# Performance work log

Hardware: AMD Instinct MI355X
Metric: run time of the kernel (lower is better)

The kernel has to match this reference:

```python
import jax, jax.numpy as jnp
import numpy as np

NUM_CLASSES = 21
THRESHOLD = 0.5
VAR0, VAR1 = 0.1, 0.2
NEGPOS_RATIO = 3


def setup_inputs() -> dict:
    key = jax.random.key(0)
    k1, k2, k3, k4, k5, k6, k7 = jax.random.split(key, 7)
    B, P, C, O = 64, 8732, 21, 8
    loc_data = jax.random.normal(k1, (B, P, 4), dtype=jnp.float32) * 0.1
    conf_data = jax.random.normal(k2, (B, P, C), dtype=jnp.float32)
    # priors: center form (cx, cy, w, h), valid in [0,1]
    cxy = jax.random.uniform(k3, (P, 2), minval=0.05, maxval=0.95)
    pwh = jax.random.uniform(k4, (P, 2), minval=0.05, maxval=0.3)
    priors = jnp.concatenate([cxy, pwh], axis=-1).astype(jnp.float32)
    # targets: corner-form boxes + class label (float), (B, O, 5)
    tc = jax.random.uniform(k5, (B, O, 2), minval=0.2, maxval=0.8)
    twh = jax.random.uniform(k6, (B, O, 2), minval=0.1, maxval=0.4)
    tmin = jnp.clip(tc - twh / 2, 0.0, 1.0)
    tmax = jnp.clip(tc + twh / 2, 0.0, 1.0)
    labels = jax.random.randint(k7, (B, O, 1), 0, C - 1).astype(jnp.float32)
    targets = jnp.concatenate([tmin, tmax, labels], axis=-1)
    return {"loc_data": loc_data, "conf_data": conf_data, "priors": priors, "targets": targets}


def _point_form(p):
    # (cx,cy,w,h) -> (xmin,ymin,xmax,ymax)
    return jnp.concatenate([p[:, :2] - p[:, 2:] / 2, p[:, :2] + p[:, 2:] / 2], axis=-1)


def _jaccard(a, b):
    # a: (O,4) corners, b: (P,4) corners -> (O,P)
    lt = jnp.maximum(a[:, None, :2], b[None, :, :2])
    rb = jnp.minimum(a[:, None, 2:], b[None, :, 2:])
    wh = jnp.clip(rb - lt, 0.0, None)
    inter = wh[..., 0] * wh[..., 1]
    area_a = ((a[:, 2] - a[:, 0]) * (a[:, 3] - a[:, 1]))[:, None]
    area_b = ((b[:, 2] - b[:, 0]) * (b[:, 3] - b[:, 1]))[None, :]
    return inter / (area_a + area_b - inter)


def _match_one(truths, labels, priors_pt, priors):
    # truths: (O,4) corners, labels: (O,), priors: (P,4) center-form
    ov = _jaccard(truths, priors_pt)                      # (O,P)
    best_prior_idx = jnp.argmax(ov, axis=1)               # (O,)
    best_truth_overlap = jnp.max(ov, axis=0)              # (P,)
    best_truth_idx = jnp.argmax(ov, axis=0)               # (P,)
    # ensure every gt box matches its best prior
    best_truth_overlap = best_truth_overlap.at[best_prior_idx].set(2.0)
    best_truth_idx = best_truth_idx.at[best_prior_idx].set(jnp.arange(truths.shape[0]))
    matched = truths[best_truth_idx]                      # (P,4)
    conf = labels[best_truth_idx].astype(jnp.int32) + 1
    conf = jnp.where(best_truth_overlap < THRESHOLD, 0, conf)
    # encode offsets
    g_cxcy = ((matched[:, :2] + matched[:, 2:]) / 2 - priors[:, :2]) / (VAR0 * priors[:, 2:])
    g_wh = jnp.log(jnp.clip((matched[:, 2:] - matched[:, :2]) / priors[:, 2:], 1e-8, None)) / VAR1
    return jnp.concatenate([g_cxcy, g_wh], axis=-1), conf


def _forward(loc_data, conf_data, priors, targets):
    B, P, C = conf_data.shape
    priors_sg = jax.lax.stop_gradient(priors)             # torch uses .data
    targets_sg = jax.lax.stop_gradient(targets)
    priors_pt = _point_form(priors_sg)
    loc_t, conf_t = jax.vmap(_match_one, in_axes=(0, 0, None, None))(
        targets_sg[:, :, :4], targets_sg[:, :, 4], priors_pt, priors_sg)
    pos = conf_t > 0                                      # (B,P)

    # localization: smooth L1 summed over positive priors
    diff = loc_data - loc_t
    ad = jnp.abs(diff)
    sl1 = jnp.where(ad < 1.0, 0.5 * diff * diff, ad - 0.5)
    loss_l = jnp.sum(sl1 * pos[..., None].astype(sl1.dtype))

    # per-prior conf loss for hard negative mining
    lse = jax.nn.logsumexp(conf_data, axis=-1)            # (B,P)
    gathered = jnp.take_along_axis(conf_data, conf_t[..., None], axis=-1)[..., 0]
    loss_c_all = lse - gathered                           # (B,P)
    mined = jnp.where(pos, 0.0, loss_c_all)
    loss_idx = jnp.argsort(-mined, axis=1)                # descending
    idx_rank = jnp.argsort(loss_idx, axis=1)
    num_pos = jnp.sum(pos.astype(jnp.int32), axis=1, keepdims=True)  # (B,1)
    num_neg = jnp.minimum(NEGPOS_RATIO * num_pos, P - num_pos)
    neg = idx_rank < num_neg                              # (B,P)

    sel = (pos | neg).astype(loss_c_all.dtype)
    loss_c = jnp.sum(loss_c_all * sel)

    N = jnp.sum(num_pos).astype(loss_l.dtype)
    return loss_l / N, loss_c / N


def reference(loc_data, conf_data, priors, targets):
    return _forward(loc_data, conf_data, priors, targets)
```

## Files before the change

### kernel.cpp

```cpp
#include <hip/hip_runtime.h>
#include <math.h>

#define TPB 256
#define TPBS 1024
#define LDSF 12288
#define HP 17

typedef unsigned long long ull;
typedef float pf4 __attribute__((ext_vector_type(4), aligned(4)));

__device__ __forceinline__ float jac(float tx0, float ty0, float tx1, float ty1, float ta,
                                     float px0, float py0, float px1, float py1, float pa) {
    float ltx = fmaxf(tx0, px0), lty = fmaxf(ty0, py0);
    float rbx = fminf(tx1, px1), rby = fminf(ty1, py1);
    float w = fmaxf(rbx - ltx, 0.0f), h = fmaxf(rby - lty, 0.0f);
    float inter = w * h;
    return inter / (ta + pa - inter);
}

template <int ON, int CN>
__global__ __launch_bounds__(TPB) void fused_kernel(
    const float* __restrict__ loc, const float* __restrict__ priors,
    const float* __restrict__ targets, const float* __restrict__ conf,
    int P, int O_rt, int C_rt, int CB2,
    float* __restrict__ mined, ull* __restrict__ pkeys,
    float* __restrict__ part_ll, float* __restrict__ part_pc,
    int* __restrict__ part_np) {
    constexpr int OMAX = (ON > 0) ? ON : 64;
    constexpr int CC = (CN > 0) ? CN : 32;
    const int O = (ON > 0) ? ON : O_rt;
    const int C = (CN > 0) ? CN : C_rt;
    const int b = blockIdx.x / CB2;
    const int chunk = blockIdx.x % CB2;
    const int tid = threadIdx.x;
    const int p = chunk * TPB + tid;
    const bool pv = (p < P);
    const int lane = tid & 63, wv = tid >> 6;

    __shared__ float s_tx0[OMAX], s_ty0[OMAX], s_tx1[OMAX], s_ty1[OMAX];
    __shared__ float s_lab[OMAX], s_area[OMAX];
    __shared__ ull s_wk[TPB / 64][OMAX];
    __shared__ float s_wll[TPB / 64], s_wpc[TPB / 64];
    __shared__ int s_wnp[TPB / 64];

    float rv[CC];
    float4 pr4 = make_float4(0.f, 0.f, 1.f, 1.f);
    if (pv) {
        const float* row = conf + ((size_t)b * P + p) * C;
        if (CN > 0) {
#pragma unroll
            for (int q = 0; q < CN / 4; ++q) {
                pf4 v = *(const pf4*)(row + 4 * q);
#pragma unroll
                for (int e = 0; e < 4; ++e) rv[4 * q + e] = v[e];
            }
#pragma unroll
            for (int j = (CN / 4) * 4; j < CN; ++j) rv[j] = row[j];
        } else {
            for (int j = 0; j < C; ++j) rv[j] = row[j];
        }
        pr4 = ((const float4*)priors)[p];
    }

    for (int o = tid; o < O; o += TPB) {
        const float* t = targets + ((size_t)b * O + o) * 5;
        float x0 = t[0], y0 = t[1], x1 = t[2], y1 = t[3];
        s_tx0[o] = x0; s_ty0[o] = y0; s_tx1[o] = x1; s_ty1[o] = y1;
        s_lab[o] = t[4];
        s_area[o] = (x1 - x0) * (y1 - y0);
    }
    __syncthreads();

    float cx = pr4.x, cy = pr4.y, pw = pr4.z, ph = pr4.w;
    float px0 = cx - pw * 0.5f, py0 = cy - ph * 0.5f;
    float px1 = cx + pw * 0.5f, py1 = cy + ph * 0.5f;
    float pa = (px1 - px0) * (py1 - py0);
    float bto = -1.0f;
    int bti = 0;
    for (int o = 0; o < O; ++o) {
        float ov = -1.0f;
        if (pv) {
            ov = jac(s_tx0[o], s_ty0[o], s_tx1[o], s_ty1[o], s_area[o],
                     px0, py0, px1, py1, pa);
            if (ov > bto) { bto = ov; bti = o; }
        }
        float mx = ov;
#pragma unroll
        for (int d = 1; d < 64; d <<= 1)
            mx = fmaxf(mx, __shfl_xor(mx, d, 64));
        ull kk = 0ull;
        if (mx >= 0.0f) {
            ull msk = __ballot(ov == mx);
            int src = __ffsll(msk) - 1;
            unsigned pw_ = (unsigned)(chunk * TPB + (wv << 6) + src);
            kk = ((ull)__float_as_uint(mx) << 32) | (ull)(0xFFFFFFFFu - pw_);
        }
        if (lane == 0) s_wk[wv][o] = kk;
    }
    __syncthreads();
    if (tid < O) {
        ull kk = s_wk[0][tid];
        for (int w = 1; w < TPB / 64; ++w)
            if (s_wk[w][tid] > kk) kk = s_wk[w][tid];
        pkeys[((size_t)b * O + tid) * CB2 + chunk] = kk;
    }

    float ll = 0.0f, pc = 0.0f;
    int np = 0;
    if (pv) {
        float m = rv[0];
#pragma unroll
        for (int j = 1; j < CC; ++j) { if (CN > 0 || j < C) m = fmaxf(m, rv[j]); }
        float s = 0.0f;
#pragma unroll
        for (int j = 0; j < CC; ++j) { if (CN > 0 || j < C) s += __expf(rv[j] - m); }
        float lse = m + __logf(s);

        int c = (bto < 0.5f) ? 0 : ((int)s_lab[bti] + 1);
        float rowc = rv[0];
#pragma unroll
        for (int j = 1; j < CC; ++j) { if (CN > 0 || j < C) { if (c == j) rowc = rv[j]; } }
        float lc = lse - rowc;

        bool pos = c > 0;
        mined[(size_t)b * P + p] = pos ? 0.0f : lc;
        if (pos) {
            pc = lc;
            np = 1;
            float mx0 = s_tx0[bti], my0 = s_ty0[bti];
            float mx1 = s_tx1[bti], my1 = s_ty1[bti];
            float g0 = ((mx0 + mx1) * 0.5f - cx) / (0.1f * pw);
            float g1 = ((my0 + my1) * 0.5f - cy) / (0.1f * ph);
            float g2 = logf(fmaxf((mx1 - mx0) / pw, 1e-8f)) / 0.2f;
            float g3 = logf(fmaxf((my1 - my0) / ph, 1e-8f)) / 0.2f;
            float4 ld = ((const float4*)loc)[(size_t)b * P + p];
            float gt4[4] = {g0, g1, g2, g3};
            float lv[4] = {ld.x, ld.y, ld.z, ld.w};
#pragma unroll
            for (int q = 0; q < 4; ++q) {
                float d = lv[q] - gt4[q];
                float ad = fabsf(d);
                ll += (ad < 1.0f) ? 0.5f * d * d : (ad - 0.5f);
            }
        }
    }

#pragma unroll
    for (int d = 1; d < 64; d <<= 1) {
        ll += __shfl_xor(ll, d, 64);
        pc += __shfl_xor(pc, d, 64);
        np += __shfl_xor(np, d, 64);
    }
    if (lane == 0) { s_wll[wv] = ll; s_wpc[wv] = pc; s_wnp[wv] = np; }
    __syncthreads();
    if (tid == 0) {
        float L = 0.f, Pc = 0.f;
        int N = 0;
        for (int w = 0; w < TPB / 64; ++w) { L += s_wll[w]; Pc += s_wpc[w]; N += s_wnp[w]; }
        part_ll[blockIdx.x] = L;
        part_pc[blockIdx.x] = Pc;
        part_np[blockIdx.x] = N;
    }
}

template <int ON, int CN>
__global__ __launch_bounds__(TPBS) void select_kernel(
    const float* __restrict__ mined, const float* __restrict__ conf,
    const float* __restrict__ loc, const float* __restrict__ priors,
    const float* __restrict__ targets, const ull* __restrict__ pkeys,
    const float* __restrict__ part_ll, const float* __restrict__ part_pc,
    const int* __restrict__ part_np,
    float* __restrict__ ll_batch, float* __restrict__ lc_batch,
    int* __restrict__ np_batch,
    int P, int O_rt, int C_rt, int CB2, int ratio) {
    constexpr int OMAX = (ON > 0) ? ON : 64;
    constexpr int NV = LDSF / TPBS;
    const int O = (ON > 0) ? ON : O_rt;
    const int C = (CN > 0) ? CN : C_rt;
    const int b = blockIdx.x, tid = threadIdx.x;
    const int lane = tid & 63, wv = tid >> 6;
    constexpr int W = TPBS / 64;
    const float* v = mined + (size_t)b * P;
    const bool reg = (P <= NV * TPBS);

    __shared__ int s_hist[256 * HP];
    __shared__ float s_tx0[OMAX], s_ty0[OMAX], s_tx1[OMAX], s_ty1[OMAX];
    __shared__ float s_lab[OMAX], s_area[OMAX];
    __shared__ ull s_keys[OMAX];
    __shared__ int s_bp[OMAX];
    __shared__ float s_wf[W], s_wg[W];
    __shared__ int s_wi[W];
    __shared__ int s_wt[4];
    __shared__ unsigned s_bsel;
    __shared__ int s_krn;
    __shared__ float s_bc[2], s_fix[2];
    __shared__ int s_bn, s_fixn;

    float val[NV];
#pragma unroll
    for (int j = 0; j < NV; ++j) {
        int i = tid + j * TPBS;
        val[j] = (reg && i < P) ? v[i] : 0.0f;
    }

    float pll = 0.0f, ppc = 0.0f;
    int pnp = 0;
    for (int i = tid; i < CB2; i += TPBS) {
        pll += part_ll[b * CB2 + i];
        ppc += part_pc[b * CB2 + i];
        pnp += part_np[b * CB2 + i];
    }
#pragma unroll
    for (int d = 1; d < 64; d <<= 1) {
        pll += __shfl_xor(pll, d, 64);
        ppc += __shfl_xor(ppc, d, 64);
        pnp += __shfl_xor(pnp, d, 64);
    }
    if (lane == 0) { s_wf[wv] = pll; s_wg[wv] = ppc; s_wi[wv] = pnp; }

    if (tid < O) {
        const float* t = targets + ((size_t)b * O + tid) * 5;
        float x0 = t[0], y0 = t[1], x1 = t[2], y1 = t[3];
        s_tx0[tid] = x0; s_ty0[tid] = y0; s_tx1[tid] = x1; s_ty1[tid] = y1;
        s_lab[tid] = t[4];
        s_area[tid] = (x1 - x0) * (y1 - y0);
        s_keys[tid] = 0ull;
    }
    __syncthreads();

    for (int i = tid; i < O * CB2; i += TPBS) {
        int o = i / CB2, s = i % CB2;
        atomicMax(&s_keys[o], pkeys[((size_t)b * O + o) * CB2 + s]);
    }
    __syncthreads();
    if (tid < O)
        s_bp[tid] = (int)(0xFFFFFFFFu - (unsigned)(s_keys[tid] & 0xFFFFFFFFull));
    __syncthreads();

    if (reg) {
#pragma unroll
        for (int j = 0; j < NV; ++j) {
            int i = tid + j * TPBS;
            bool z = false;
            for (int o = 0; o < O; ++o) z |= (s_bp[o] == i);
            if (z) val[j] = 0.0f;
        }
    }
    unsigned uvv[NV];
#pragma unroll
    for (int j = 0; j < NV; ++j) uvv[j] = __float_as_uint(val[j]);

    float dll = 0.0f, dpc = 0.0f;
    int dnp = 0;
    if (tid < O) {
        const int o = tid;
        const int p = s_bp[o];
        bool owner = true;
        for (int o2 = o + 1; o2 < O; ++o2)
            if (s_bp[o2] == p) owner = false;
        if (owner) {
            float4 pr = ((const float4*)priors)[p];
            float cx = pr.x, cy = pr.y, pw = pr.z, ph = pr.w;
            float px0 = cx - pw * 0.5f, py0 = cy - ph * 0.5f;
            float px1 = cx + pw * 0.5f, py1 = cy + ph * 0.5f;
            float pa = (px1 - px0) * (py1 - py0);
            float bto = -1.0f;
            int bti = 0;
            for (int o2 = 0; o2 < O; ++o2) {
                float ov = jac(s_tx0[o2], s_ty0[o2], s_tx1[o2], s_ty1[o2], s_area[o2],
                               px0, py0, px1, py1, pa);
                if (ov > bto) { bto = ov; bti = o2; }
            }
            int c_t = (bto < 0.5f) ? 0 : ((int)s_lab[bti] + 1);
            const float* row = conf + ((size_t)b * P + p) * C;
            float m = row[0];
            for (int j = 1; j < C; ++j) m = fmaxf(m, row[j]);
            float s = 0.0f;
            for (int j = 0; j < C; ++j) s += __expf(row[j] - m);
            float lse = m + __logf(s);
            int c_n = (int)s_lab[o] + 1;
            float lc_n = lse - row[c_n];
            bool pos_t = c_t > 0;
            float lc_t = lse - row[c_t];
            dpc = lc_n - (pos_t ? lc_t : 0.0f);
            dnp = 1 - (pos_t ? 1 : 0);
            float4 ld = ((const float4*)loc)[(size_t)b * P + p];
            float lv[4] = {ld.x, ld.y, ld.z, ld.w};
            float sl_new = 0.0f, sl_old = 0.0f;
            {
                float mx0 = s_tx0[o], my0 = s_ty0[o], mx1 = s_tx1[o], my1 = s_ty1[o];
                float g[4] = {((mx0 + mx1) * 0.5f - cx) / (0.1f * pw),
                              ((my0 + my1) * 0.5f - cy) / (0.1f * ph),
                              logf(fmaxf((mx1 - mx0) / pw, 1e-8f)) / 0.2f,
                              logf(fmaxf((my1 - my0) / ph, 1e-8f)) / 0.2f};
                for (int q = 0; q < 4; ++q) {
                    float d = lv[q] - g[q];
                    float ad = fabsf(d);
                    sl_new += (ad < 1.0f) ? 0.5f * d * d : (ad - 0.5f);
                }
            }
            if (pos_t) {
                float mx0 = s_tx0[bti], my0 = s_ty0[bti], mx1 = s_tx1[bti], my1 = s_ty1[bti];
                float g[4] = {((mx0 + mx1) * 0.5f - cx) / (0.1f * pw),
                              ((my0 + my1) * 0.5f - cy) / (0.1f * ph),
                              logf(fmaxf((mx1 - mx0) / pw, 1e-8f)) / 0.2f,
                              logf(fmaxf((my1 - my0) / ph, 1e-8f)) / 0.2f};
                for (int q = 0; q < 4; ++q) {
                    float d = lv[q] - g[q];
                    float ad = fabsf(d);
                    sl_old += (ad < 1.0f) ? 0.5f * d * d : (ad - 0.5f);
                }
            }
            dll = sl_new - sl_old;
        }
    }
    if (wv == 0) {
#pragma unroll
        for (int d = 1; d < 64; d <<= 1) {
            dll += __shfl_xor(dll, d, 64);
            dpc += __shfl_xor(dpc, d, 64);
            dnp += __shfl_xor(dnp, d, 64);
        }
        if (lane == 0) { s_fix[0] = dll; s_fix[1] = dpc; s_fixn = dnp; }
    }
    __syncthreads();
    if (tid == 0) {
        float L = 0.f, Pc = 0.f;
        int N = 0;
        for (int w = 0; w < W; ++w) { L += s_wf[w]; Pc += s_wg[w]; N += s_wi[w]; }
        s_bc[0] = L + s_fix[0]; s_bc[1] = Pc + s_fix[1]; s_bn = N + s_fixn;
    }
    __syncthreads();
    const float ll_sum = s_bc[0];
    const float sum_pos = s_bc[1];
    const int npos = s_bn;

    const int k = min(ratio * npos, P - npos);
    if (tid == 0) {
        ll_batch[b] = ll_sum;
        np_batch[b] = npos;
    }
    if (k <= 0) {
        if (tid == 0) lc_batch[b] = sum_pos;
        return;
    }

    unsigned prefix = 0u;
    int kr = k;
    for (int pass = 0; pass < 4; ++pass) {
        const int shift = 24 - 8 * pass;
        const unsigned mask = (pass == 0) ? 0u : (0xFFFFFFFFu << (32 - 8 * pass));
        for (int i = tid; i < 256 * HP; i += TPBS) s_hist[i] = 0;
        __syncthreads();
        if (reg) {
#pragma unroll
            for (int j = 0; j < NV; ++j) {
                int i = tid + j * TPBS;
                unsigned u = uvv[j];
                bool match = (i < P) && ((u & mask) == prefix);
                int bin = (u >> shift) & 0xFF;
                if (pass == 0) {
                    ull act = __ballot(match);
                    while (act) {
                        int src = __ffsll(act) - 1;
                        int b0 = __shfl(bin, src, 64);
                        ull same = __ballot(match && bin == b0) & act;
                        if (lane == src)
                            atomicAdd(&s_hist[b0 * HP + wv], (int)__popcll(same));
                        act &= ~same;
                    }
                } else if (match) {
                    atomicAdd(&s_hist[bin * HP + wv], 1);
                }
            }
        } else {
            for (int i = tid; i < P; i += TPBS) {
                float x = v[i];
                for (int o = 0; o < O; ++o)
                    if (i == s_bp[o]) x = 0.0f;
                unsigned u = __float_as_uint(x);
                bool match = ((u & mask) == prefix);
                int bin = (u >> shift) & 0xFF;
                if (pass == 0) {
                    ull act = __ballot(match);
                    while (act) {
                        int src = __ffsll(act) - 1;
                        int b0 = __shfl(bin, src, 64);
                        ull same = __ballot(match && bin == b0) & act;
                        if (lane == src)
                            atomicAdd(&s_hist[b0 * HP + wv], (int)__popcll(same));
                        act &= ~same;
                    }
                } else if (match) {
                    atomicAdd(&s_hist[bin * HP + wv], 1);
                }
            }
        }
        __syncthreads();
        int sge = 0, h = 0;
        if (tid < 256) {
            for (int w = 0; w < W; ++w) h += s_hist[tid * HP + w];
            int val_ = h;
#pragma unroll
            for (int d = 1; d < 64; d <<= 1) {
                int t = __shfl_down(val_, d, 64);
                if (lane + d < 64) val_ += t;
            }
            if (lane == 0) s_wt[tid >> 6] = val_;
            sge = val_;
        }
        __syncthreads();
        if (tid < 256) {
            for (int w = (tid >> 6) + 1; w < 4; ++w) sge += s_wt[w];
            int sgt = sge - h;
            if (sge >= kr && sgt < kr) {
                s_bsel = (unsigned)tid;
                s_krn = kr - sgt;
            }
        }
        __syncthreads();
        prefix |= s_bsel << shift;
        kr = s_krn;
    }
    const float T = __uint_as_float(prefix);
    float lsum = 0.0f;
    int lcnt = 0;
    if (reg) {
#pragma unroll
        for (int j = 0; j < NV; ++j) {
            int i = tid + j * TPBS;
            if (i < P && val[j] > T) { lsum += val[j]; ++lcnt; }
        }
    } else {
        for (int i = tid; i < P; i += TPBS) {
            float x = v[i];
            for (int o = 0; o < O; ++o)
                if (i == s_bp[o]) x = 0.0f;
            if (x > T) { lsum += x; ++lcnt; }
        }
    }
#pragma unroll
    for (int d = 1; d < 64; d <<= 1) {
        lsum += __shfl_xor(lsum, d, 64);
        lcnt += __shfl_xor(lcnt, d, 64);
    }
    if (lane == 0) { s_wf[wv] = lsum; s_wi[wv] = lcnt; }
    __syncthreads();
    if (tid == 0) {
        float S = 0.f;
        int Cn = 0;
        for (int w = 0; w < W; ++w) { S += s_wf[w]; Cn += s_wi[w]; }
        lc_batch[b] = sum_pos + S + (float)(k - Cn) * T;
    }
}

__global__ __launch_bounds__(TPB) void finalize_kernel(
    const float* __restrict__ ll_batch, const int* __restrict__ np_batch,
    const float* __restrict__ lc_batch, int B, float* __restrict__ out) {
    const int tid = threadIdx.x;
    __shared__ float s_l[TPB], s_c[TPB];
    __shared__ int s_n[TPB];
    float l = 0.0f, c = 0.0f;
    int n = 0;
    for (int i = tid; i < B; i += TPB) {
        l += ll_batch[i];
        c += lc_batch[i];
        n += np_batch[i];
    }
    s_l[tid] = l; s_c[tid] = c; s_n[tid] = n;
    __syncthreads();
    for (int s = TPB / 2; s > 0; s >>= 1) {
        if (tid < s) {
            s_l[tid] += s_l[tid + s];
            s_c[tid] += s_c[tid + s];
            s_n[tid] += s_n[tid + s];
        }
        __syncthreads();
    }
    if (tid == 0) {
        float N = (float)s_n[0];
        out[0] = s_l[0] / N;
        out[1] = s_c[0] / N;
    }
}

extern "C" void kernel_launch(void* const* d_in, const int* in_sizes, int n_in,
                              void* d_out, int out_size, void* d_ws, size_t ws_size,
                              hipStream_t stream) {
    const float* loc = (const float*)d_in[0];
    const float* conf = (const float*)d_in[1];
    const float* priors = (const float*)d_in[2];
    const float* targets = (const float*)d_in[3];

    const int P = in_sizes[2] / 4;
    const int B = in_sizes[0] / (P * 4);
    const int C = in_sizes[1] / (in_sizes[0] / 4);
    const int O = in_sizes[3] / (B * 5);
    const size_t BP = (size_t)B * P;
    const int CB2 = (P + TPB - 1) / TPB;

    ull* pkeys = (ull*)d_ws;
    float* mined = (float*)(pkeys + (size_t)B * O * CB2);
    float* part_ll = mined + BP;
    float* part_pc = part_ll + (size_t)B * CB2;
    int* part_np = (int*)(part_pc + (size_t)B * CB2);
    float* ll_batch = (float*)(part_np + (size_t)B * CB2);
    float* lc_batch = ll_batch + B;
    int* np_batch = (int*)(lc_batch + B);

    if (O == 8 && C == 21) {
        fused_kernel<8, 21><<<B * CB2, TPB, 0, stream>>>(
            loc, priors, targets, conf, P, O, C, CB2,
            mined, pkeys, part_ll, part_pc, part_np);
        select_kernel<8, 21><<<B, TPBS, 0, stream>>>(
            mined, conf, loc, priors, targets, pkeys, part_ll, part_pc, part_np,
            ll_batch, lc_batch, np_batch, P, O, C, CB2, 3);
    } else {
        fused_kernel<0, 0><<<B * CB2, TPB, 0, stream>>>(
            loc, priors, targets, conf, P, O, C, CB2,
            mined, pkeys, part_ll, part_pc, part_np);
        select_kernel<0, 0><<<B, TPBS, 0, stream>>>(
            mined, conf, loc, priors, targets, pkeys, part_ll, part_pc, part_np,
            ll_batch, lc_batch, np_batch, P, O, C, CB2, 3);
    }

    finalize_kernel<<<1, TPB, 0, stream>>>(ll_batch, np_batch, lc_batch, B,
                                           (float*)d_out);
}
```

Measured before the change: 118.8 us.

## Build first radix-select histogram in fused kernel and drop block key reduction

The fused kernel now builds the top-byte histogram of the mined loss for each 256-prior chunk. It packs each histogram as 16-bit pairs into a workspace buffer, and the select kernel sums these instead of doing pass 0 over all priors. Forced-match priors are fixed up in the histogram by moving one count to bin 0. The per-block max reduction of match keys is also removed: each wave writes its key directly and select reduces four times as many entries. Register-held values shrink from 12 to 9 per thread, and the per-wave padded histogram becomes a single shared histogram. This trades a 1024-thread serial pass for more global partial data and a CB2-long serial loop in select.

Result: no change. 117.9 us (-0.8%).

```diff
diff --git a/kernel.cpp b/kernel.cpp
--- a/kernel.cpp
+++ b/kernel.cpp
@@ -3,8 +3,7 @@
 
 #define TPB 256
 #define TPBS 1024
-#define LDSF 12288
-#define HP 17
+#define NVREG 9
 
 typedef unsigned long long ull;
 typedef float pf4 __attribute__((ext_vector_type(4), aligned(4)));
@@ -25,9 +24,10 @@
     int P, int O_rt, int C_rt, int CB2,
     float* __restrict__ mined, ull* __restrict__ pkeys,
     float* __restrict__ part_ll, float* __restrict__ part_pc,
-    int* __restrict__ part_np) {
+    int* __restrict__ part_np, unsigned* __restrict__ chist) {
     constexpr int OMAX = (ON > 0) ? ON : 64;
     constexpr int CC = (CN > 0) ? CN : 32;
+    constexpr int WPB = TPB / 64;
     const int O = (ON > 0) ? ON : O_rt;
     const int C = (CN > 0) ? CN : C_rt;
     const int b = blockIdx.x / CB2;
@@ -36,12 +36,13 @@
     const int p = chunk * TPB + tid;
     const bool pv = (p < P);
     const int lane = tid & 63, wv = tid >> 6;
+    const int CB2W = CB2 * WPB;
 
     __shared__ float s_tx0[OMAX], s_ty0[OMAX], s_tx1[OMAX], s_ty1[OMAX];
     __shared__ float s_lab[OMAX], s_area[OMAX];
-    __shared__ ull s_wk[TPB / 64][OMAX];
-    __shared__ float s_wll[TPB / 64], s_wpc[TPB / 64];
-    __shared__ int s_wnp[TPB / 64];
+    __shared__ int s_h[256];
+    __shared__ float s_wll[WPB], s_wpc[WPB];
+    __shared__ int s_wnp[WPB];
 
     float rv[CC];
     float4 pr4 = make_float4(0.f, 0.f, 1.f, 1.f);
@@ -62,6 +63,7 @@
         pr4 = ((const float4*)priors)[p];
     }
 
+    s_h[tid] = 0;
     for (int o = tid; o < O; o += TPB) {
         const float* t = targets + ((size_t)b * O + o) * 5;
         float x0 = t[0], y0 = t[1], x1 = t[2], y1 = t[3];
@@ -95,18 +97,14 @@
             unsigned pw_ = (unsigned)(chunk * TPB + (wv << 6) + src);
             kk = ((ull)__float_as_uint(mx) << 32) | (ull)(0xFFFFFFFFu - pw_);
         }
-        if (lane == 0) s_wk[wv][o] = kk;
-    }
-    __syncthreads();
-    if (tid < O) {
-        ull kk = s_wk[0][tid];
-        for (int w = 1; w < TPB / 64; ++w)
-            if (s_wk[w][tid] > kk) kk = s_wk[w][tid];
-        pkeys[((size_t)b * O + tid) * CB2 + chunk] = kk;
+        if (lane == 0)
+            pkeys[((size_t)b * O + o) * CB2W + chunk * WPB + wv] = kk;
     }
 
     float ll = 0.0f, pc = 0.0f;
     int np = 0;
+    int bin = 0;
+    bool hv = false;
     if (pv) {
         float m = rv[0];
 #pragma unroll
@@ -123,7 +121,10 @@
         float lc = lse - rowc;
 
         bool pos = c > 0;
-        mined[(size_t)b * P + p] = pos ? 0.0f : lc;
+        float mv = pos ? 0.0f : lc;
+        mined[(size_t)b * P + p] = mv;
+        bin = (int)(__float_as_uint(mv) >> 24);
+        hv = true;
         if (pos) {
             pc = lc;
             np = 1;
@@ -145,6 +146,17 @@
         }
     }
 
+    {
+        ull act = __ballot(hv);
+        while (act) {
+            int src = __ffsll(act) - 1;
+            int b0 = __shfl(bin, src, 64);
+            ull same = __ballot(hv && bin == b0) & act;
+            if (lane == src) atomicAdd(&s_h[b0], (int)__popcll(same));
+            act &= ~same;
+        }
+    }
+
 #pragma unroll
     for (int d = 1; d < 64; d <<= 1) {
         ll += __shfl_xor(ll, d, 64);
@@ -156,10 +168,14 @@
     if (tid == 0) {
         float L = 0.f, Pc = 0.f;
         int N = 0;
-        for (int w = 0; w < TPB / 64; ++w) { L += s_wll[w]; Pc += s_wpc[w]; N += s_wnp[w]; }
+        for (int w = 0; w < WPB; ++w) { L += s_wll[w]; Pc += s_wpc[w]; N += s_wnp[w]; }
         part_ll[blockIdx.x] = L;
         part_pc[blockIdx.x] = Pc;
         part_np[blockIdx.x] = N;
+    }
+    if (tid < 128) {
+        unsigned wd = (unsigned)s_h[2 * tid] | ((unsigned)s_h[2 * tid + 1] << 16);
+        chist[((size_t)b * CB2 + chunk) * 128 + tid] = wd;
     }
 }
 
@@ -169,21 +185,22 @@
     const float* __restrict__ loc, const float* __restrict__ priors,
     const float* __restrict__ targets, const ull* __restrict__ pkeys,
     const float* __restrict__ part_ll, const float* __restrict__ part_pc,
-    const int* __restrict__ part_np,
+    const int* __restrict__ part_np, const unsigned* __restrict__ chist,
     float* __restrict__ ll_batch, float* __restrict__ lc_batch,
     int* __restrict__ np_batch,
     int P, int O_rt, int C_rt, int CB2, int ratio) {
     constexpr int OMAX = (ON > 0) ? ON : 64;
-    constexpr int NV = LDSF / TPBS;
+    constexpr int NV = NVREG;
     const int O = (ON > 0) ? ON : O_rt;
     const int C = (CN > 0) ? CN : C_rt;
     const int b = blockIdx.x, tid = threadIdx.x;
     const int lane = tid & 63, wv = tid >> 6;
     constexpr int W = TPBS / 64;
+    const int CB2W = CB2 * (TPB / 64);
     const float* v = mined + (size_t)b * P;
     const bool reg = (P <= NV * TPBS);
 
-    __shared__ int s_hist[256 * HP];
+    __shared__ int s_hist[256];
     __shared__ float s_tx0[OMAX], s_ty0[OMAX], s_tx1[OMAX], s_ty1[OMAX];
     __shared__ float s_lab[OMAX], s_area[OMAX];
     __shared__ ull s_keys[OMAX];
@@ -228,9 +245,9 @@
     }
     __syncthreads();
 
-    for (int i = tid; i < O * CB2; i += TPBS) {
-        int o = i / CB2, s = i % CB2;
-        atomicMax(&s_keys[o], pkeys[((size_t)b * O + o) * CB2 + s]);
+    for (int i = tid; i < O * CB2W; i += TPBS) {
+        int o = i / CB2W, s = i % CB2W;
+        atomicMax(&s_keys[o], pkeys[((size_t)b * O + o) * CB2W + s]);
     }
     __syncthreads();
     if (tid < O)
@@ -250,8 +267,17 @@
 #pragma unroll
     for (int j = 0; j < NV; ++j) uvv[j] = __float_as_uint(val[j]);
 
+    if (tid < 256) {
+        int h = 0;
+        const unsigned* cb = chist + (size_t)b * CB2 * 128 + (tid >> 1);
+        const int sh = (tid & 1) * 16;
+        for (int c = 0; c < CB2; ++c) h += (int)((cb[c * 128] >> sh) & 0xFFFFu);
+        s_hist[tid] = h;
+    }
+
     float dll = 0.0f, dpc = 0.0f;
     int dnp = 0;
+    int adj_bin = -1;
     if (tid < O) {
         const int o = tid;
         const int p = s_bp[o];
@@ -259,6 +285,7 @@
         for (int o2 = o + 1; o2 < O; ++o2)
             if (s_bp[o2] == p) owner = false;
         if (owner) {
+            adj_bin = (int)(__float_as_uint(v[p]) >> 24);
             float4 pr = ((const float4*)priors)[p];
             float cx = pr.x, cy = pr.y, pw = pr.z, ph = pr.w;
             float px0 = cx - pw * 0.5f, py0 = cy - ph * 0.5f;
@@ -324,6 +351,10 @@
         if (lane == 0) { s_fix[0] = dll; s_fix[1] = dpc; s_fixn = dnp; }
     }
     __syncthreads();
+    if (adj_bin > 0) {
+        atomicAdd(&s_hist[adj_bin], -1);
+        atomicAdd(&s_hist[0], 1);
+    }
     if (tid == 0) {
         float L = 0.f, Pc = 0.f;
         int N = 0;
@@ -349,57 +380,33 @@
     int kr = k;
     for (int pass = 0; pass < 4; ++pass) {
         const int shift = 24 - 8 * pass;
-        const unsigned mask = (pass == 0) ? 0u : (0xFFFFFFFFu << (32 - 8 * pass));
-        for (int i = tid; i < 256 * HP; i += TPBS) s_hist[i] = 0;
-        __syncthreads();
-        if (reg) {
-#pragma unroll
-            for (int j = 0; j < NV; ++j) {
-                int i = tid + j * TPBS;
-                unsigned u = uvv[j];
-                bool match = (i < P) && ((u & mask) == prefix);
-                int bin = (u >> shift) & 0xFF;
-                if (pass == 0) {
-                    ull act = __ballot(match);
-                    while (act) {
-                        int src = __ffsll(act) - 1;
-                        int b0 = __shfl(bin, src, 64);
-                        ull same = __ballot(match && bin == b0) & act;
-                        if (lane == src)
-                            atomicAdd(&s_hist[b0 * HP + wv], (int)__popcll(same));
-                        act &= ~same;
-                    }
-                } else if (match) {
-                    atomicAdd(&s_hist[bin * HP + wv], 1);
+        if (pass > 0) {
+            const unsigned mask = 0xFFFFFFFFu << (32 - 8 * pass);
+            if (tid < 256) s_hist[tid] = 0;
+            __syncthreads();
+            if (reg) {
+#pragma unroll
+                for (int j = 0; j < NV; ++j) {
+                    int i = tid + j * TPBS;
+                    unsigned u = uvv[j];
+                    if (i < P && (u & mask) == prefix)
+                        atomicAdd(&s_hist[(u >> shift) & 0xFF], 1);
                 }
-            }
-        } else {
-            for (int i = tid; i < P; i += TPBS) {
-                float x = v[i];
-                for (int o = 0; o < O; ++o)
-                    if (i == s_bp[o]) x = 0.0f;
-                unsigned u = __float_as_uint(x);
-                bool match = ((u & mask) == prefix);
-                int bin = (u >> shift) & 0xFF;
-                if (pass == 0) {
-                    ull act = __ballot(match);
-                    while (act) {
-                        int src = __ffsll(act) - 1;
-                        int b0 = __shfl(bin, src, 64);
-                        ull same = __ballot(match && bin == b0) & act;
-                        if (lane == src)
-                            atomicAdd(&s_hist[b0 * HP + wv], (int)__popcll(same));
-                        act &= ~same;
-                    }
-                } else if (match) {
-                    atomicAdd(&s_hist[bin * HP + wv], 1);
+            } else {
+                for (int i = tid; i < P; i += TPBS) {
+                    float x = v[i];
+                    for (int o = 0; o < O; ++o)
+                        if (i == s_bp[o]) x = 0.0f;
+                    unsigned u = __float_as_uint(x);
+                    if ((u & mask) == prefix)
+                        atomicAdd(&s_hist[(u >> shift) & 0xFF], 1);
                 }
             }
-        }
-        __syncthreads();
+            __syncthreads();
+        }
         int sge = 0, h = 0;
         if (tid < 256) {
-            for (int w = 0; w < W; ++w) h += s_hist[tid * HP + w];
+            h = s_hist[tid];
             int val_ = h;
 #pragma unroll
             for (int d = 1; d < 64; d <<= 1) {
@@ -498,30 +505,32 @@
     const int O = in_sizes[3] / (B * 5);
     const size_t BP = (size_t)B * P;
     const int CB2 = (P + TPB - 1) / TPB;
+    const int CB2W = CB2 * (TPB / 64);
 
     ull* pkeys = (ull*)d_ws;
-    float* mined = (float*)(pkeys + (size_t)B * O * CB2);
+    float* mined = (float*)(pkeys + (size_t)B * O * CB2W);
     float* part_ll = mined + BP;
     float* part_pc = part_ll + (size_t)B * CB2;
     int* part_np = (int*)(part_pc + (size_t)B * CB2);
-    float* ll_batch = (float*)(part_np + (size_t)B * CB2);
+    unsigned* chist = (unsigned*)(part_np + (size_t)B * CB2);
+    float* ll_batch = (float*)(chist + (size_t)B * CB2 * 128);
     float* lc_batch = ll_batch + B;
     int* np_batch = (int*)(lc_batch + B);
 
     if (O == 8 && C == 21) {
         fused_kernel<8, 21><<<B * CB2, TPB, 0, stream>>>(
             loc, priors, targets, conf, P, O, C, CB2,
-            mined, pkeys, part_ll, part_pc, part_np);
+            mined, pkeys, part_ll, part_pc, part_np, chist);
         select_kernel<8, 21><<<B, TPBS, 0, stream>>>(
             mined, conf, loc, priors, targets, pkeys, part_ll, part_pc, part_np,
-            ll_batch, lc_batch, np_batch, P, O, C, CB2, 3);
+            chist, ll_batch, lc_batch, np_batch, P, O, C, CB2, 3);
     } else {
         fused_kernel<0, 0><<<B * CB2, TPB, 0, stream>>>(
             loc, priors, targets, conf, P, O, C, CB2,
-            mined, pkeys, part_ll, part_pc, part_np);
+            mined, pkeys, part_ll, part_pc, part_np, chist);
         select_kernel<0, 0><<<B, TPBS, 0, stream>>>(
             mined, conf, loc, priors, targets, pkeys, part_ll, part_pc, part_np,
-            ll_batch, lc_batch, np_batch, P, O, C, CB2, 3);
+            chist, ll_batch, lc_batch, np_batch, P, O, C, CB2, 3);
     }
 
     finalize_kernel<<<1, TPB, 0, stream>>>(ll_batch, np_batch, lc_batch, B,
```
